# Optimization experiments

Hardware: AMD Instinct MI355X
Metric: run time of the kernel (lower is better)

The kernel has to match this reference:

```python
import jax, jax.numpy as jnp
import numpy as np

BN_EPS = 1e-5


def setup_inputs() -> dict:
    key = jax.random.key(0)
    ks = jax.random.split(key, 4)
    S, B, F, P, T, H, W = 4, 2, 64, 16, 32, 64, 64
    HID = 32
    feats = jax.random.normal(ks[0], (S, B, F, T, H, W), dtype=jnp.float32)
    p_s = jax.random.normal(ks[1], (B, P, T, H, W), dtype=jnp.float32)
    w1 = jax.random.normal(ks[2], (HID, F + P), dtype=jnp.float32) * (1.0 / np.sqrt(F + P))
    w2 = jax.random.normal(ks[3], (HID,), dtype=jnp.float32) * (1.0 / np.sqrt(HID))
    return {
        "feats": feats,
        "p_s": p_s,
        "w1": w1,
        "bn_gamma": jnp.ones((HID,), jnp.float32),
        "bn_beta": jnp.zeros((HID,), jnp.float32),
        "bn_mean": jnp.zeros((HID,), jnp.float32),
        "bn_var": jnp.ones((HID,), jnp.float32),
        "w2": w2,
        "b2": jnp.zeros((1,), jnp.float32),
    }


def reference(feats, p_s, w1, bn_gamma, bn_beta, bn_mean, bn_var, w2, b2):
    # feats: [S,B,F,T,H,W]; p_s: [B,P,T,H,W]
    F = feats.shape[2]
    w1_f, w1_p = w1[:, :F], w1[:, F:]
    # 1x1x1 conv on concat([f, p_s]) == split contraction; avoids materializing concat
    h = jnp.einsum('of,sbfthw->sbothw', w1_f, feats) \
        + jnp.einsum('op,bpthw->bothw', w1_p, p_s)[None]
    # BatchNorm3d (inference form) folded to scale/shift, then ReLU
    scale = bn_gamma / jnp.sqrt(bn_var + BN_EPS)
    shift = bn_beta - bn_mean * scale
    h = jax.nn.relu(h * scale[:, None, None, None] + shift[:, None, None, None])
    # second 1x1x1 conv: hidden -> 1 logit per branch
    logits = jnp.einsum('sbothw,o->sbthw', h, w2) + b2[0]
    alpha = jax.nn.softmax(logits, axis=0)            # softmax over branches S
    out = jnp.einsum('sbfthw,sbthw->bfthw', feats, alpha)
    return out, jnp.moveaxis(alpha, 0, 1)             # out:[B,F,T,H,W], alpha:[B,S,T,H,W]
```

## Files before the change

kernel.cpp:

```cpp
#include <hip/hip_runtime.h>
#include <hip/hip_bf16.h>
#include <stdint.h>

#define THW   131072
#define NS    4
#define NB    2
#define NF    64
#define NP    16
#define HID   32
#define BN_EPS 1e-5f

typedef short  bf16x8  __attribute__((ext_vector_type(8)));
typedef float  f32x16  __attribute__((ext_vector_type(16)));

union FragU { uint32_t u[4]; bf16x8 v; };

__device__ __forceinline__ uint32_t pack_bf16(float a, float b) {
    uint32_t ua = __builtin_bit_cast(uint32_t, a);
    uint32_t ub = __builtin_bit_cast(uint32_t, b);
    ua = (ua + 0x7FFFu + ((ua >> 16) & 1u)) >> 16;
    ub = (ub + 0x7FFFu + ((ub >> 16) & 1u)) >> 16;
    return ua | (ub << 16);
}

__global__ __launch_bounds__(256, 2) void gssm_kernel(
    const float* __restrict__ feats, const float* __restrict__ ps,
    const float* __restrict__ w1,    const float* __restrict__ gamma,
    const float* __restrict__ beta,  const float* __restrict__ mean,
    const float* __restrict__ var,   const float* __restrict__ w2,
    float* __restrict__ out)
{
    __shared__ float4 tbl[HID];
    const int tid = threadIdx.x;
    if (tid < HID) {
        float sc = gamma[tid] * rsqrtf(var[tid] + BN_EPS);
        float sh = beta[tid] - mean[tid] * sc;
        tbl[tid] = make_float4(sc, sh, w2[tid], 0.f);
    }
    __syncthreads();

    const int lane = tid & 63;
    const int wv   = tid >> 6;
    const int hi   = lane >> 5;
    const int ln   = lane & 31;

    const int tile = blockIdx.x * 4 + wv;
    const int pix0 = tile * 32;
    const int b    = pix0 >> 17;
    const int thw  = (pix0 & (THW - 1)) + ln;

    FragU afr[5];
    #pragma unroll
    for (int k = 0; k < 5; ++k) {
        const float* wrow = w1 + ln * (NF + NP) + k * 16 + hi * 8;
        #pragma unroll
        for (int r = 0; r < 4; ++r)
            afr[k].u[r] = pack_bf16(wrow[2 * r], wrow[2 * r + 1]);
    }

    f32x16 accp;
    #pragma unroll
    for (int r = 0; r < 16; ++r) accp[r] = 0.f;
    {
        FragU bp;
        const float* pb = ps + ((long)(b * NP + hi * 8)) * THW + thw;
        #pragma unroll
        for (int r = 0; r < 4; ++r)
            bp.u[r] = pack_bf16(pb[(long)(2 * r) * THW], pb[(long)(2 * r + 1) * THW]);
        accp = __builtin_amdgcn_mfma_f32_32x32x16_bf16(afr[4].v, bp.v, accp, 0, 0, 0);
    }

    float num[32];
    #pragma unroll
    for (int i = 0; i < 32; ++i) num[i] = 0.f;
    float mrun = -1e30f, den = 0.f;
    float logits[4];

    #pragma unroll
    for (int s = 0; s < NS; ++s) {
        float fv[32];
        const float* fb = feats + ((long)((s * NB + b) * NF + hi * 8)) * THW + thw;
        #pragma unroll
        for (int k = 0; k < 4; ++k)
            #pragma unroll
            for (int j = 0; j < 8; ++j)
                fv[k * 8 + j] = fb[(long)(k * 16 + j) * THW];

        f32x16 acc = accp;
        #pragma unroll
        for (int k = 0; k < 4; ++k) {
            FragU bf;
            #pragma unroll
            for (int r = 0; r < 4; ++r)
                bf.u[r] = pack_bf16(fv[k * 8 + 2 * r], fv[k * 8 + 2 * r + 1]);
            acc = __builtin_amdgcn_mfma_f32_32x32x16_bf16(afr[k].v, bf.v, acc, 0, 0, 0);
        }

        float part = 0.f;
        #pragma unroll
        for (int r = 0; r < 16; ++r) {
            const int row = (r & 3) + 8 * (r >> 2) + 4 * hi;
            float4 t = tbl[row];
            float h = fmaxf(fmaf(acc[r], t.x, t.y), 0.f);
            part = fmaf(h, t.z, part);
        }
        const float logit = part + __shfl_xor(part, 32);
        logits[s] = logit;

        const float mn  = fmaxf(mrun, logit);
        const float rsc = __expf(mrun - mn);
        const float e   = __expf(logit - mn);
        den = den * rsc + e;
        #pragma unroll
        for (int i = 0; i < 32; ++i)
            num[i] = fmaf(num[i], rsc, e * fv[i]);
        mrun = mn;
    }

    const float inv = 1.f / den;

    float* ob = out + ((long)(b * NF + hi * 8)) * THW + thw;
    #pragma unroll
    for (int k = 0; k < 4; ++k)
        #pragma unroll
        for (int j = 0; j < 8; ++j)
            ob[(long)(k * 16 + j) * THW] = num[k * 8 + j] * inv;

    float* ab = out + (long)NB * NF * THW + ((long)(b * NS + hi * 2)) * THW + thw;
    ab[0]   = __expf(logits[2 * hi]     - mrun) * inv;
    ab[THW] = __expf(logits[2 * hi + 1] - mrun) * inv;
}

extern "C" void kernel_launch(void* const* d_in, const int* in_sizes, int n_in,
                              void* d_out, int out_size, void* d_ws, size_t ws_size,
                              hipStream_t stream) {
    const float* feats = (const float*)d_in[0];
    const float* ps    = (const float*)d_in[1];
    const float* w1    = (const float*)d_in[2];
    const float* gamma = (const float*)d_in[3];
    const float* beta  = (const float*)d_in[4];
    const float* mean  = (const float*)d_in[5];
    const float* var   = (const float*)d_in[6];
    const float* w2    = (const float*)d_in[7];
    float* out = (float*)d_out;

    dim3 grid(2048), block(256);
    hipLaunchKernelGGL(gssm_kernel, grid, block, 0, stream,
                       feats, ps, w1, gamma, beta, mean, var, w2, out);
}
```

Baseline: 95.78 us.

## Stage bf16 w1 in LDS and keep feats packed to raise occupancy

Converts w1 to bf16 once per block into padded LDS and reads MFMA A-fragments from there, instead of holding five fragments in registers. Feats are kept only as packed bf16 pairs and unpacked for the softmax-weighted sum, and the p_s contribution is recomputed per branch. Together these cut register pressure so launch bounds can request four blocks per SM instead of two, improving memory latency hiding. The weighted output now uses bf16-rounded features, adding precision loss to the output.

```diff
diff --git a/kernel.cpp b/kernel.cpp
--- a/kernel.cpp
+++ b/kernel.cpp
@@ -13,25 +13,32 @@
 typedef short  bf16x8  __attribute__((ext_vector_type(8)));
 typedef float  f32x16  __attribute__((ext_vector_type(16)));
 
-union FragU { uint32_t u[4]; bf16x8 v; };
+union FragU { uint32_t u[4]; bf16x8 v; uint4 q; };
 
-__device__ __forceinline__ uint32_t pack_bf16(float a, float b) {
-    uint32_t ua = __builtin_bit_cast(uint32_t, a);
-    uint32_t ub = __builtin_bit_cast(uint32_t, b);
-    ua = (ua + 0x7FFFu + ((ua >> 16) & 1u)) >> 16;
-    ub = (ub + 0x7FFFu + ((ub >> 16) & 1u)) >> 16;
-    return ua | (ub << 16);
+__device__ __forceinline__ uint32_t pk2(float a, float b) {
+    __hip_bfloat162 h = __float22bfloat162_rn(make_float2(a, b));
+    uint32_t r;
+    __builtin_memcpy(&r, &h, sizeof(r));
+    return r;
 }
 
-__global__ __launch_bounds__(256, 2) void gssm_kernel(
+__global__ __launch_bounds__(256, 4) void gssm_kernel(
     const float* __restrict__ feats, const float* __restrict__ ps,
     const float* __restrict__ w1,    const float* __restrict__ gamma,
     const float* __restrict__ beta,  const float* __restrict__ mean,
     const float* __restrict__ var,   const float* __restrict__ w2,
     float* __restrict__ out)
 {
+    __shared__ __align__(16) uint32_t w1lds[32 * 44];
     __shared__ float4 tbl[HID];
+
     const int tid = threadIdx.x;
+    for (int t = tid; t < 1280; t += 256) {
+        float2 v = ((const float2*)w1)[t];
+        int o = t / 40, cp = t - o * 40;
+        int k = cp >> 3, rem = cp & 7;
+        w1lds[o * 44 + k * 8 + rem] = pk2(v.x, v.y);
+    }
     if (tid < HID) {
         float sc = gamma[tid] * rsqrtf(var[tid] + BN_EPS);
         float sh = beta[tid] - mean[tid] * sc;
@@ -49,51 +56,52 @@
     const int b    = pix0 >> 17;
     const int thw  = (pix0 & (THW - 1)) + ln;
 
-    FragU afr[5];
-    #pragma unroll
-    for (int k = 0; k < 5; ++k) {
-        const float* wrow = w1 + ln * (NF + NP) + k * 16 + hi * 8;
+    const uint32_t abase = (uint32_t)(ln * 44 + hi * 4);
+
+    FragU bp;
+    {
+        const float* pb = ps + ((long)(b * NP + hi * 8)) * THW + thw;
+        float pv[8];
         #pragma unroll
-        for (int r = 0; r < 4; ++r)
-            afr[k].u[r] = pack_bf16(wrow[2 * r], wrow[2 * r + 1]);
-    }
-
-    f32x16 accp;
-    #pragma unroll
-    for (int r = 0; r < 16; ++r) accp[r] = 0.f;
-    {
-        FragU bp;
-        const float* pb = ps + ((long)(b * NP + hi * 8)) * THW + thw;
+        for (int r = 0; r < 8; ++r) pv[r] = pb[(long)r * THW];
         #pragma unroll
-        for (int r = 0; r < 4; ++r)
-            bp.u[r] = pack_bf16(pb[(long)(2 * r) * THW], pb[(long)(2 * r + 1) * THW]);
-        accp = __builtin_amdgcn_mfma_f32_32x32x16_bf16(afr[4].v, bp.v, accp, 0, 0, 0);
+        for (int r = 0; r < 4; ++r) bp.u[r] = pk2(pv[2 * r], pv[2 * r + 1]);
     }
 
     float num[32];
     #pragma unroll
     for (int i = 0; i < 32; ++i) num[i] = 0.f;
     float mrun = -1e30f, den = 0.f;
-    float logits[4];
+    float lg[4];
 
     #pragma unroll
     for (int s = 0; s < NS; ++s) {
-        float fv[32];
         const float* fb = feats + ((long)((s * NB + b) * NF + hi * 8)) * THW + thw;
+
+        FragU pkk[4];
         #pragma unroll
-        for (int k = 0; k < 4; ++k)
+        for (int k = 0; k < 4; ++k) {
+            float fv[8];
             #pragma unroll
             for (int j = 0; j < 8; ++j)
-                fv[k * 8 + j] = fb[(long)(k * 16 + j) * THW];
+                fv[j] = fb[(long)(k * 16 + j) * THW];
+            #pragma unroll
+            for (int r = 0; r < 4; ++r)
+                pkk[k].u[r] = pk2(fv[2 * r], fv[2 * r + 1]);
+        }
 
-        f32x16 acc = accp;
+        f32x16 acc;
+        #pragma unroll
+        for (int r = 0; r < 16; ++r) acc[r] = 0.f;
+
+        {
+            FragU af; af.q = *((const uint4*)&w1lds[abase + 4 * 8]);
+            acc = __builtin_amdgcn_mfma_f32_32x32x16_bf16(af.v, bp.v, acc, 0, 0, 0);
+        }
         #pragma unroll
         for (int k = 0; k < 4; ++k) {
-            FragU bf;
-            #pragma unroll
-            for (int r = 0; r < 4; ++r)
-                bf.u[r] = pack_bf16(fv[k * 8 + 2 * r], fv[k * 8 + 2 * r + 1]);
-            acc = __builtin_amdgcn_mfma_f32_32x32x16_bf16(afr[k].v, bf.v, acc, 0, 0, 0);
+            FragU af; af.q = *((const uint4*)&w1lds[abase + k * 8]);
+            acc = __builtin_amdgcn_mfma_f32_32x32x16_bf16(af.v, pkk[k].v, acc, 0, 0, 0);
         }
 
         float part = 0.f;
@@ -105,15 +113,21 @@
             part = fmaf(h, t.z, part);
         }
         const float logit = part + __shfl_xor(part, 32);
-        logits[s] = logit;
+        lg[s] = logit;
 
         const float mn  = fmaxf(mrun, logit);
         const float rsc = __expf(mrun - mn);
         const float e   = __expf(logit - mn);
         den = den * rsc + e;
         #pragma unroll
-        for (int i = 0; i < 32; ++i)
-            num[i] = fmaf(num[i], rsc, e * fv[i]);
+        for (int k = 0; k < 4; ++k)
+            #pragma unroll
+            for (int r = 0; r < 4; ++r) {
+                const float flo = __builtin_bit_cast(float, pkk[k].u[r] << 16);
+                const float fhi = __builtin_bit_cast(float, pkk[k].u[r] & 0xFFFF0000u);
+                num[k * 8 + 2 * r]     = fmaf(num[k * 8 + 2 * r],     rsc, e * flo);
+                num[k * 8 + 2 * r + 1] = fmaf(num[k * 8 + 2 * r + 1], rsc, e * fhi);
+            }
         mrun = mn;
     }
 
@@ -126,9 +140,11 @@
         for (int j = 0; j < 8; ++j)
             ob[(long)(k * 16 + j) * THW] = num[k * 8 + j] * inv;
 
+    const float la = hi ? lg[2] : lg[0];
+    const float lb = hi ? lg[3] : lg[1];
     float* ab = out + (long)NB * NF * THW + ((long)(b * NS + hi * 2)) * THW + thw;
-    ab[0]   = __expf(logits[2 * hi]     - mrun) * inv;
-    ab[THW] = __expf(logits[2 * hi + 1] - mrun) * inv;
+    ab[0]   = __expf(la - mrun) * inv;
+    ab[THW] = __expf(lb - mrun) * inv;
 }
 
 extern "C" void kernel_launch(void* const* d_in, const int* in_sizes, int n_in,
```

Measured after the change: 152.9 us. 59.7% more time.
